# Kernel tuning notes

Hardware: AMD Instinct MI355X
Metric: run time of the kernel (lower is better)

## Reference

```python
import jax, jax.numpy as jnp
import numpy as np

KH, KW = 7, 7          # neighborhood kernel
NH = 8                 # num heads
PAD = (KW - 1) // 2    # circular pad along width


def setup_inputs() -> dict:
    key = jax.random.key(0)
    ks = jax.random.split(key, 6)
    B, H, W, C = 1, 180, 360, 256
    x = jax.random.normal(ks[0], (B, H, W, C), dtype=jnp.float32)
    w_qkv = jax.random.normal(ks[1], (C, 3 * C), dtype=jnp.float32) * 0.02
    b_qkv = jnp.zeros((3 * C,), dtype=jnp.float32)
    rpb = jax.random.normal(ks[2], (NH, 2 * KH - 1, 2 * KW - 1), dtype=jnp.float32) * 0.02
    w_proj = jax.random.normal(ks[3], (C, C), dtype=jnp.float32) * 0.02
    b_proj = jnp.zeros((C,), dtype=jnp.float32)
    return {"x": x, "w_qkv": w_qkv, "b_qkv": b_qkv, "rpb": rpb,
            "w_proj": w_proj, "b_proj": b_proj}


def _na2d(x, w_qkv, b_qkv, rpb, w_proj, b_proj):
    # x: [B, H, W, C] (already circularly padded along W)
    B, H, W, C = x.shape
    d = C // NH
    scale = d ** -0.5
    qkv = x @ w_qkv + b_qkv                       # [B,H,W,3C]
    qkv = qkv.reshape(B, H, W, 3, NH, d).transpose(3, 0, 4, 1, 2, 5)
    q, k, v = qkv[0] * scale, qkv[1], qkv[2]      # each [B,NH,H,W,d]

    # natten window start (clamped so the k x k window stays in-bounds)
    start_h = jnp.clip(jnp.arange(H) - (KH - 1) // 2, 0, H - KH)   # [H]
    start_w = jnp.clip(jnp.arange(W) - (KW - 1) // 2, 0, W - KW)   # [W]
    rel_h0 = start_h - jnp.arange(H) + (KH - 1)   # rpb row index base
    rel_w0 = start_w - jnp.arange(W) + (KW - 1)   # rpb col index base

    # scan over the KH*KW kernel offsets (honors the local-window sparsity;
    # never materializes [H,W,KH,KW,d] windows)
    oi, oj = jnp.meshgrid(jnp.arange(KH), jnp.arange(KW), indexing="ij")
    offs = jnp.stack([oi.ravel(), oj.ravel()], axis=-1)           # [KH*KW, 2]

    def score_body(_, off):
        kk = jnp.take(jnp.take(k, start_h + off[0], axis=2), start_w + off[1], axis=3)
        s = jnp.einsum("bnhwd,bnhwd->bnhw", q, kk)                # [B,NH,H,W]
        bias = rpb[:, rel_h0 + off[0], :][:, :, rel_w0 + off[1]]  # [NH,H,W]
        return None, s + bias[None]

    _, scores = jax.lax.scan(score_body, None, offs)              # [KH*KW,B,NH,H,W]
    attn = jax.nn.softmax(scores, axis=0)

    def out_body(acc, t):
        off, a = t
        vv = jnp.take(jnp.take(v, start_h + off[0], axis=2), start_w + off[1], axis=3)
        return acc + a[..., None] * vv, None

    out, _ = jax.lax.scan(out_body, jnp.zeros(q.shape, q.dtype), (offs, attn))
    out = out.transpose(0, 2, 3, 1, 4).reshape(B, H, W, C)        # merge heads
    return out @ w_proj + b_proj


def reference(x, w_qkv, b_qkv, rpb, w_proj, b_proj):
    # circular pad along width, neighborhood attention, crop back
    xp = jnp.pad(x, ((0, 0), (0, 0), (PAD, PAD), (0, 0)), mode="wrap")
    out = _na2d(xp, w_qkv, b_qkv, rpb, w_proj, b_proj)
    return out[:, :, PAD:out.shape[2] - PAD, :]
```

## Files before the change

### kernel.cpp

```cpp
#include <hip/hip_runtime.h>
#include <hip/hip_fp16.h>
#include <math.h>

#define H_DIM 180
#define W_DIM 360
#define CH    256
#define NHEAD 8
#define HD    32
#define MPIX  (H_DIM * W_DIM)
#define KDIM  256

typedef _Float16 f16x8 __attribute__((ext_vector_type(8)));
typedef _Float16 h2    __attribute__((ext_vector_type(2)));
typedef float    f32x4 __attribute__((ext_vector_type(4)));

#if __has_builtin(__builtin_amdgcn_fdot2)
#define HAS_FDOT2 1
#else
#define HAS_FDOT2 0
#endif

__device__ __forceinline__ h2 pack2(float a, float b) {
#if __has_builtin(__builtin_amdgcn_cvt_pkrtz)
    return __builtin_bit_cast(h2, __builtin_amdgcn_cvt_pkrtz(a, b));
#else
    h2 r; r.x = (_Float16)a; r.y = (_Float16)b; return r;
#endif
}

__global__ __launch_bounds__(256)
void convert_kernel(const float* __restrict__ X, const float* __restrict__ Wq,
                    const float* __restrict__ Wp, _Float16* __restrict__ Xh,
                    _Float16* __restrict__ Wqt, _Float16* __restrict__ Wpt)
{
    const int tid = blockIdx.x * 256 + threadIdx.x;
    if (blockIdx.y == 0) {
        const float4* X4 = reinterpret_cast<const float4*>(X);
        const float4 a = X4[tid * 2];
        const float4 b = X4[tid * 2 + 1];
        uint4 o;
        o.x = __builtin_bit_cast(unsigned, pack2(a.x, a.y));
        o.y = __builtin_bit_cast(unsigned, pack2(a.z, a.w));
        o.z = __builtin_bit_cast(unsigned, pack2(b.x, b.y));
        o.w = __builtin_bit_cast(unsigned, pack2(b.z, b.w));
        reinterpret_cast<uint4*>(Xh)[tid] = o;
    } else if (blockIdx.y == 1) {
        if (tid < 768 * 256) {
            const int n = tid >> 8, k = tid & 255;
            Wqt[tid] = (_Float16)Wq[k * 768 + n];
        }
    } else {
        if (tid < 256 * 256) {
            const int n = tid >> 8, k = tid & 255;
            Wpt[tid] = (_Float16)Wp[k * 256 + n];
        }
    }
}

template<int NB, int MODE>
__global__ __launch_bounds__(256)
void mfma_gemm_kernel(const _Float16* __restrict__ A,
                      const _Float16* __restrict__ Bt,
                      const float* __restrict__ bias,
                      _Float16* __restrict__ qo, _Float16* __restrict__ ko,
                      _Float16* __restrict__ vo, float* __restrict__ outf,
                      int M)
{
    __shared__ __align__(16) _Float16 Alds[128 * 64];
    __shared__ __align__(16) _Float16 Blds[128 * 64];

    const int tid  = threadIdx.x;
    const int wid  = tid >> 6;
    const int lane = tid & 63;
    const int bn   = blockIdx.x * 128;
    const int bm   = blockIdx.y * 128;
    const int wr   = wid >> 1;
    const int wc   = wid & 1;

    f32x4 acc[4][4] = {};

    const int srow  = lane >> 3;
    const int sunit = (lane & 7) * 16;

    for (int k0 = 0; k0 < KDIM; k0 += 64) {
        #pragma unroll
        for (int i = 0; i < 4; ++i) {
            const int chunk = i * 4 + wid;
            const int row   = chunk * 8 + srow;
            int am = bm + row;
            am = (am < M) ? am : (M - 1);
            const char* asrc = (const char*)(A + (size_t)am * KDIM + k0) + sunit;
            __builtin_amdgcn_global_load_lds(
                (const __attribute__((address_space(1))) void*)asrc,
                (__attribute__((address_space(3))) void*)((char*)Alds + chunk * 1024),
                16, 0, 0);
            const char* bsrc = (const char*)(Bt + (size_t)(bn + row) * KDIM + k0) + sunit;
            __builtin_amdgcn_global_load_lds(
                (const __attribute__((address_space(1))) void*)bsrc,
                (__attribute__((address_space(3))) void*)((char*)Blds + chunk * 1024),
                16, 0, 0);
        }
        __syncthreads();
        #pragma unroll
        for (int kk = 0; kk < 64; kk += 32) {
            const int ko2 = kk + (lane >> 4) * 8;
            f16x8 af[4], bf[4];
            #pragma unroll
            for (int t = 0; t < 4; ++t) {
                af[t] = *(const f16x8*)&Alds[(wr * 64 + t * 16 + (lane & 15)) * 64 + ko2];
                bf[t] = *(const f16x8*)&Blds[(wc * 64 + t * 16 + (lane & 15)) * 64 + ko2];
            }
            #pragma unroll
            for (int fi = 0; fi < 4; ++fi)
                #pragma unroll
                for (int fj = 0; fj < 4; ++fj)
                    acc[fi][fj] = __builtin_amdgcn_mfma_f32_16x16x32_f16(
                        af[fi], bf[fj], acc[fi][fj], 0, 0, 0);
        }
        __syncthreads();
    }

    const int lc  = lane & 15;
    const int lrb = (lane >> 4) * 4;
    if (MODE == 0) {
        const float scale = 0.17677669529663687f;
        _Float16* sw = Alds + wid * 640;
        const int row = lane >> 2;
        const int seg = lane & 3;
        #pragma unroll
        for (int fi = 0; fi < 4; ++fi) {
            #pragma unroll
            for (int fp = 0; fp < 2; ++fp) {
                #pragma unroll
                for (int ff = 0; ff < 2; ++ff) {
                    const int fj = fp * 2 + ff;
                    const int c = bn + wc * 64 + fj * 16 + lc;
                    const float bv = bias[c];
                    const float scl = ((c >> 8) == 0) ? scale : 1.0f;
                    #pragma unroll
                    for (int j = 0; j < 4; ++j)
                        sw[(lrb + j) * 34 + ff * 16 + lc] =
                            (_Float16)((acc[fi][fj][j] + bv) * scl);
                }
                const int c0 = bn + wc * 64 + fp * 32;
                const int which = c0 >> 8;
                const int head  = (c0 >> 5) & 7;
                _Float16* dst = (which == 0) ? qo : (which == 1) ? ko : vo;
                const int m = bm + wr * 64 + fi * 16 + row;
                f16x8 vv = *(const f16x8*)&sw[row * 34 + seg * 8];
                if (m < M)
                    *(f16x8*)&dst[((size_t)head * M + m) * HD + seg * 8] = vv;
            }
        }
    } else {
        #pragma unroll
        for (int fj = 0; fj < 4; ++fj) {
            const int c = bn + wc * 64 + fj * 16 + lc;
            const float bv = bias[c];
            #pragma unroll
            for (int fi = 0; fi < 4; ++fi) {
                #pragma unroll
                for (int j = 0; j < 4; ++j) {
                    const int m = bm + wr * 64 + fi * 16 + lrb + j;
                    if (m < M)
                        outf[(size_t)m * NB + c] = acc[fi][fj][j] + bv;
                }
            }
        }
    }
}

#define KROWS 14
#define KCOLS 38
#define KUNITS (KROWS * KCOLS * 4)
#define KUNITS_PAD 2304

__device__ __forceinline__ void stage_dma(const uint4* __restrict__ src,
                                          uint4* __restrict__ dstlds,
                                          int n, int r0, int w0, int tid)
{
    const int wid  = tid >> 6;
    const int lane = tid & 63;
    #pragma unroll
    for (int it = 0; it < 9; ++it) {
        const int u0 = it * 256 + wid * 64;
        const int u  = u0 + lane;
        const int row = u / (KCOLS * 4);
        const int rem = u - row * (KCOLS * 4);
        const int t   = rem / KCOLS;
        const int col = rem - t * KCOLS;
        int grow = r0 + row;
        if (grow > H_DIM - 1) grow = H_DIM - 1;
        int gcol = w0 - 3 + col;
        if (gcol < 0) gcol += W_DIM;
        else if (gcol >= W_DIM) gcol -= W_DIM;
        const size_t gidx = (((size_t)n * H_DIM + grow) * W_DIM + gcol) * 4 + t;
        __builtin_amdgcn_global_load_lds(
            (const __attribute__((address_space(1))) void*)(src + gidx),
            (__attribute__((address_space(3))) void*)(dstlds + u0), 16, 0, 0);
    }
}

__global__ __launch_bounds__(256)
void natten_attn_kernel(const _Float16* __restrict__ q,
                        const uint4* __restrict__ kb,
                        const uint4* __restrict__ vb,
                        const float* __restrict__ rpb,
                        _Float16* __restrict__ outh)
{
    __shared__ uint4 kvs[KUNITS_PAD];
    __shared__ float rpbs[169];

    const int tid = threadIdx.x;
    const int n  = blockIdx.z;
    const int w0 = blockIdx.x * 32;
    const int h0 = blockIdx.y * 8;

    int r0 = h0 - 3;
    if (r0 < 0) r0 = 0;
    if (r0 > H_DIM - 7) r0 = H_DIM - 7;

    if (tid < 169) rpbs[tid] = rpb[n * 169 + tid];

    const int hl = tid >> 5;
    const int wl = tid & 31;
    const int h = h0 + hl;
    const int w = w0 + wl;
    const bool valid = (h < H_DIM) && (w < W_DIM);

    const int ha = (h < H_DIM) ? h : H_DIM - 1;
    const int wa = (w < W_DIM) ? w : W_DIM - 1;
    const uint4* qp = reinterpret_cast<const uint4*>(
        q + ((size_t)n * MPIX + (size_t)ha * W_DIM + wa) * HD);
    uint4 q0 = qp[0], q1 = qp[1], q2 = qp[2], q3 = qp[3];

    stage_dma(kb, kvs, n, r0, w0, tid);
    __syncthreads();

    h2 qh[16];
    qh[0]  = __builtin_bit_cast(h2, q0.x); qh[1]  = __builtin_bit_cast(h2, q0.y);
    qh[2]  = __builtin_bit_cast(h2, q0.z); qh[3]  = __builtin_bit_cast(h2, q0.w);
    qh[4]  = __builtin_bit_cast(h2, q1.x); qh[5]  = __builtin_bit_cast(h2, q1.y);
    qh[6]  = __builtin_bit_cast(h2, q1.z); qh[7]  = __builtin_bit_cast(h2, q1.w);
    qh[8]  = __builtin_bit_cast(h2, q2.x); qh[9]  = __builtin_bit_cast(h2, q2.y);
    qh[10] = __builtin_bit_cast(h2, q2.z); qh[11] = __builtin_bit_cast(h2, q2.w);
    qh[12] = __builtin_bit_cast(h2, q3.x); qh[13] = __builtin_bit_cast(h2, q3.y);
    qh[14] = __builtin_bit_cast(h2, q3.z); qh[15] = __builtin_bit_cast(h2, q3.w);

    float sc[49];
    int ri0 = 0;

    if (valid) {
        int sh = h - 3;
        if (sh < 0) sh = 0;
        if (sh > H_DIM - 7) sh = H_DIM - 7;
        ri0 = sh - r0;
        const int rh0 = sh - h + 6;

        #pragma unroll
        for (int oi = 0; oi < 7; ++oi) {
            const int rb = (ri0 + oi) * (KCOLS * 4);
            #pragma unroll
            for (int oj = 0; oj < 7; ++oj) {
                const int base = rb + wl + oj;
                float d0 = 0.f, d1 = 0.f, d2 = 0.f, d3 = 0.f;
                const uint4 ku0 = kvs[base];
                const uint4 ku1 = kvs[base + KCOLS];
                const uint4 ku2 = kvs[base + 2 * KCOLS];
                const uint4 ku3 = kvs[base + 3 * KCOLS];
#if HAS_FDOT2
                d0 = __builtin_amdgcn_fdot2(__builtin_bit_cast(h2, ku0.x), qh[0],  d0, false);
                d1 = __builtin_amdgcn_fdot2(__builtin_bit_cast(h2, ku1.x), qh[4],  d1, false);
                d2 = __builtin_amdgcn_fdot2(__builtin_bit_cast(h2, ku2.x), qh[8],  d2, false);
                d3 = __builtin_amdgcn_fdot2(__builtin_bit_cast(h2, ku3.x), qh[12], d3, false);
                d0 = __builtin_amdgcn_fdot2(__builtin_bit_cast(h2, ku0.y), qh[1],  d0, false);
                d1 = __builtin_amdgcn_fdot2(__builtin_bit_cast(h2, ku1.y), qh[5],  d1, false);
                d2 = __builtin_amdgcn_fdot2(__builtin_bit_cast(h2, ku2.y), qh[9],  d2, false);
                d3 = __builtin_amdgcn_fdot2(__builtin_bit_cast(h2, ku3.y), qh[13], d3, false);
                d0 = __builtin_amdgcn_fdot2(__builtin_bit_cast(h2, ku0.z), qh[2],  d0, false);
                d1 = __builtin_amdgcn_fdot2(__builtin_bit_cast(h2, ku1.z), qh[6],  d1, false);
                d2 = __builtin_amdgcn_fdot2(__builtin_bit_cast(h2, ku2.z), qh[10], d2, false);
                d3 = __builtin_amdgcn_fdot2(__builtin_bit_cast(h2, ku3.z), qh[14], d3, false);
                d0 = __builtin_amdgcn_fdot2(__builtin_bit_cast(h2, ku0.w), qh[3],  d0, false);
                d1 = __builtin_amdgcn_fdot2(__builtin_bit_cast(h2, ku1.w), qh[7],  d1, false);
                d2 = __builtin_amdgcn_fdot2(__builtin_bit_cast(h2, ku2.w), qh[11], d2, false);
                d3 = __builtin_amdgcn_fdot2(__builtin_bit_cast(h2, ku3.w), qh[15], d3, false);
#else
                {
                    h2 a, b;
                    a = __builtin_bit_cast(h2, ku0.x); b = qh[0];
                    d0 += (float)a.x * (float)b.x + (float)a.y * (float)b.y;
                    a = __builtin_bit_cast(h2, ku0.y); b = qh[1];
                    d0 += (float)a.x * (float)b.x + (float)a.y * (float)b.y;
                    a = __builtin_bit_cast(h2, ku0.z); b = qh[2];
                    d0 += (float)a.x * (float)b.x + (float)a.y * (float)b.y;
                    a = __builtin_bit_cast(h2, ku0.w); b = qh[3];
                    d0 += (float)a.x * (float)b.x + (float)a.y * (float)b.y;
                    a = __builtin_bit_cast(h2, ku1.x); b = qh[4];
                    d1 += (float)a.x * (float)b.x + (float)a.y * (float)b.y;
                    a = __builtin_bit_cast(h2, ku1.y); b = qh[5];
                    d1 += (float)a.x * (float)b.x + (float)a.y * (float)b.y;
                    a = __builtin_bit_cast(h2, ku1.z); b = qh[6];
                    d1 += (float)a.x * (float)b.x + (float)a.y * (float)b.y;
                    a = __builtin_bit_cast(h2, ku1.w); b = qh[7];
                    d1 += (float)a.x * (float)b.x + (float)a.y * (float)b.y;
                    a = __builtin_bit_cast(h2, ku2.x); b = qh[8];
                    d2 += (float)a.x * (float)b.x + (float)a.y * (float)b.y;
                    a = __builtin_bit_cast(h2, ku2.y); b = qh[9];
                    d2 += (float)a.x * (float)b.x + (float)a.y * (float)b.y;
                    a = __builtin_bit_cast(h2, ku2.z); b = qh[10];
                    d2 += (float)a.x * (float)b.x + (float)a.y * (float)b.y;
                    a = __builtin_bit_cast(h2, ku2.w); b = qh[11];
                    d2 += (float)a.x * (float)b.x + (float)a.y * (float)b.y;
                    a = __builtin_bit_cast(h2, ku3.x); b = qh[12];
                    d3 += (float)a.x * (float)b.x + (float)a.y * (float)b.y;
                    a = __builtin_bit_cast(h2, ku3.y); b = qh[13];
                    d3 += (float)a.x * (float)b.x + (float)a.y * (float)b.y;
                    a = __builtin_bit_cast(h2, ku3.z); b = qh[14];
                    d3 += (float)a.x * (float)b.x + (float)a.y * (float)b.y;
                    a = __builtin_bit_cast(h2, ku3.w); b = qh[15];
                    d3 += (float)a.x * (float)b.x + (float)a.y * (float)b.y;
                }
#endif
                sc[oi * 7 + oj] = ((d0 + d1) + (d2 + d3))
                                + rpbs[(rh0 + oi) * 13 + 3 + oj];
            }
        }
    }
    __syncthreads();

    stage_dma(vb, kvs, n, r0, w0, tid);

    float inv = 0.f;
    if (valid) {
        float ssum = 0.f;
        #pragma unroll
        for (int i = 0; i < 49; ++i) { sc[i] = __expf(sc[i]); ssum += sc[i]; }
        inv = 1.f / ssum;
    }
    __syncthreads();

    if (!valid) return;

    float acc[32];
    #pragma unroll
    for (int t = 0; t < 32; ++t) acc[t] = 0.f;
    #pragma unroll
    for (int oi = 0; oi < 7; ++oi) {
        const int rb = (ri0 + oi) * (KCOLS * 4);
        #pragma unroll
        for (int oj = 0; oj < 7; ++oj) {
            const int base = rb + wl + oj;
            const float a = sc[oi * 7 + oj];
            #pragma unroll
            for (int t = 0; t < 4; ++t) {
                const uint4 vv = kvs[base + t * KCOLS];
                h2 v0 = __builtin_bit_cast(h2, vv.x);
                h2 v1 = __builtin_bit_cast(h2, vv.y);
                h2 v2 = __builtin_bit_cast(h2, vv.z);
                h2 v3 = __builtin_bit_cast(h2, vv.w);
                acc[t*8+0] += a * (float)v0.x; acc[t*8+1] += a * (float)v0.y;
                acc[t*8+2] += a * (float)v1.x; acc[t*8+3] += a * (float)v1.y;
                acc[t*8+4] += a * (float)v2.x; acc[t*8+5] += a * (float)v2.y;
                acc[t*8+6] += a * (float)v3.x; acc[t*8+7] += a * (float)v3.y;
            }
        }
    }

    uint4 o[4];
    #pragma unroll
    for (int t = 0; t < 4; ++t) {
        h2 p0 = { (_Float16)(acc[t*8+0] * inv), (_Float16)(acc[t*8+1] * inv) };
        h2 p1 = { (_Float16)(acc[t*8+2] * inv), (_Float16)(acc[t*8+3] * inv) };
        h2 p2 = { (_Float16)(acc[t*8+4] * inv), (_Float16)(acc[t*8+5] * inv) };
        h2 p3 = { (_Float16)(acc[t*8+6] * inv), (_Float16)(acc[t*8+7] * inv) };
        o[t].x = __builtin_bit_cast(unsigned, p0);
        o[t].y = __builtin_bit_cast(unsigned, p1);
        o[t].z = __builtin_bit_cast(unsigned, p2);
        o[t].w = __builtin_bit_cast(unsigned, p3);
    }
    uint4* op = reinterpret_cast<uint4*>(
        outh + (((size_t)h * W_DIM + w) * CH + n * HD));
    #pragma unroll
    for (int t = 0; t < 4; ++t) op[t] = o[t];
}

extern "C" void kernel_launch(void* const* d_in, const int* in_sizes, int n_in,
                              void* d_out, int out_size, void* d_ws, size_t ws_size,
                              hipStream_t stream)
{
    const float* x      = (const float*)d_in[0];
    const float* w_qkv  = (const float*)d_in[1];
    const float* b_qkv  = (const float*)d_in[2];
    const float* rpb    = (const float*)d_in[3];
    const float* w_proj = (const float*)d_in[4];
    const float* b_proj = (const float*)d_in[5];
    float* out = (float*)d_out;

    const int M = MPIX;
    const size_t nelem = (size_t)M * KDIM;

    _Float16* Xh  = (_Float16*)d_ws;
    _Float16* Wqt = Xh  + nelem;
    _Float16* Wpt = Wqt + 768 * 256;
    _Float16* qb  = Wpt + 256 * 256;
    _Float16* kb  = qb  + nelem;
    _Float16* vb  = kb  + nelem;
    _Float16* ah  = vb  + nelem;

    const size_t need = (5 * nelem + 768 * 256 + 256 * 256) * sizeof(_Float16);
    if (ws_size < need) return;

    dim3 blk(256);
    convert_kernel<<<dim3(8100, 3), blk, 0, stream>>>(x, w_qkv, w_proj, Xh, Wqt, Wpt);

    mfma_gemm_kernel<768, 0><<<dim3(6, 507), blk, 0, stream>>>(
        Xh, Wqt, b_qkv, qb, kb, vb, nullptr, M);

    natten_attn_kernel<<<dim3(12, 23, NHEAD), blk, 0, stream>>>(
        qb, (const uint4*)kb, (const uint4*)vb, rpb, ah);

    mfma_gemm_kernel<256, 1><<<dim3(2, 507), blk, 0, stream>>>(
        ah, Wpt, b_proj, nullptr, nullptr, nullptr, out, M);
}
```

Before: 197.9 us.

## Use square 16x16 attention tiles, fuse exp into scoring, pack scores to fp16

Changes the neighborhood-attention block tile from 8x32 to 16x16 pixels, which shrinks the staged K/V halo from 14x38 to 22x22 columns and cuts redundant LDS loads. The exponentials are computed inline during scoring and stored as packed fp16 pairs, which lowers register pressure, and the launch bounds now request 5 blocks per CU to raise occupancy. The trade-off is lower precision for the unnormalized softmax weights in fp16, plus a DMA loop whose last chunk overlaps the previous one.

```diff
diff --git a/kernel.cpp b/kernel.cpp
--- a/kernel.cpp
+++ b/kernel.cpp
@@ -170,10 +170,9 @@
     }
 }
 
-#define KROWS 14
-#define KCOLS 38
-#define KUNITS (KROWS * KCOLS * 4)
-#define KUNITS_PAD 2304
+#define KR 22
+#define KC 22
+#define KU (KR * KC * 4)
 
 __device__ __forceinline__ void stage_dma(const uint4* __restrict__ src,
                                           uint4* __restrict__ dstlds,
@@ -182,13 +181,14 @@
     const int wid  = tid >> 6;
     const int lane = tid & 63;
     #pragma unroll
-    for (int it = 0; it < 9; ++it) {
-        const int u0 = it * 256 + wid * 64;
+    for (int it = 0; it < 8; ++it) {
+        const int cb = (it == 7) ? (KU - 256) : it * 256;
+        const int u0 = cb + wid * 64;
         const int u  = u0 + lane;
-        const int row = u / (KCOLS * 4);
-        const int rem = u - row * (KCOLS * 4);
-        const int t   = rem / KCOLS;
-        const int col = rem - t * KCOLS;
+        const int row = u / (KC * 4);
+        const int rem = u - row * (KC * 4);
+        const int t   = rem / KC;
+        const int col = rem - t * KC;
         int grow = r0 + row;
         if (grow > H_DIM - 1) grow = H_DIM - 1;
         int gcol = w0 - 3 + col;
@@ -201,20 +201,20 @@
     }
 }
 
-__global__ __launch_bounds__(256)
+__global__ __launch_bounds__(256, 5)
 void natten_attn_kernel(const _Float16* __restrict__ q,
                         const uint4* __restrict__ kb,
                         const uint4* __restrict__ vb,
                         const float* __restrict__ rpb,
                         _Float16* __restrict__ outh)
 {
-    __shared__ uint4 kvs[KUNITS_PAD];
+    __shared__ uint4 kvs[KU];
     __shared__ float rpbs[169];
 
     const int tid = threadIdx.x;
     const int n  = blockIdx.z;
-    const int w0 = blockIdx.x * 32;
-    const int h0 = blockIdx.y * 8;
+    const int w0 = blockIdx.x * 16;
+    const int h0 = blockIdx.y * 16;
 
     int r0 = h0 - 3;
     if (r0 < 0) r0 = 0;
@@ -222,8 +222,8 @@
 
     if (tid < 169) rpbs[tid] = rpb[n * 169 + tid];
 
-    const int hl = tid >> 5;
-    const int wl = tid & 31;
+    const int hl = tid >> 4;
+    const int wl = tid & 15;
     const int h = h0 + hl;
     const int w = w0 + wl;
     const bool valid = (h < H_DIM) && (w < W_DIM);
@@ -247,7 +247,8 @@
     qh[12] = __builtin_bit_cast(h2, q3.x); qh[13] = __builtin_bit_cast(h2, q3.y);
     qh[14] = __builtin_bit_cast(h2, q3.z); qh[15] = __builtin_bit_cast(h2, q3.w);
 
-    float sc[49];
+    h2 sch[25];
+    float ssum = 0.f;
     int ri0 = 0;
 
     if (valid) {
@@ -257,17 +258,19 @@
         ri0 = sh - r0;
         const int rh0 = sh - h + 6;
 
+        float pend = 0.f;
         #pragma unroll
         for (int oi = 0; oi < 7; ++oi) {
-            const int rb = (ri0 + oi) * (KCOLS * 4);
+            const int rb = (ri0 + oi) * (KC * 4);
             #pragma unroll
             for (int oj = 0; oj < 7; ++oj) {
+                const int i = oi * 7 + oj;
                 const int base = rb + wl + oj;
                 float d0 = 0.f, d1 = 0.f, d2 = 0.f, d3 = 0.f;
                 const uint4 ku0 = kvs[base];
-                const uint4 ku1 = kvs[base + KCOLS];
-                const uint4 ku2 = kvs[base + 2 * KCOLS];
-                const uint4 ku3 = kvs[base + 3 * KCOLS];
+                const uint4 ku1 = kvs[base + KC];
+                const uint4 ku2 = kvs[base + 2 * KC];
+                const uint4 ku3 = kvs[base + 3 * KC];
 #if HAS_FDOT2
                 d0 = __builtin_amdgcn_fdot2(__builtin_bit_cast(h2, ku0.x), qh[0],  d0, false);
                 d1 = __builtin_amdgcn_fdot2(__builtin_bit_cast(h2, ku1.x), qh[4],  d1, false);
@@ -322,22 +325,21 @@
                     d3 += (float)a.x * (float)b.x + (float)a.y * (float)b.y;
                 }
 #endif
-                sc[oi * 7 + oj] = ((d0 + d1) + (d2 + d3))
-                                + rpbs[(rh0 + oi) * 13 + 3 + oj];
+                const float s = ((d0 + d1) + (d2 + d3))
+                              + rpbs[(rh0 + oi) * 13 + 3 + oj];
+                const float e = __expf(s);
+                ssum += e;
+                if (i & 1) sch[i >> 1] = pack2(pend, e);
+                else       pend = e;
             }
         }
+        sch[24] = pack2(pend, 0.f);
     }
     __syncthreads();
 
     stage_dma(vb, kvs, n, r0, w0, tid);
-
     float inv = 0.f;
-    if (valid) {
-        float ssum = 0.f;
-        #pragma unroll
-        for (int i = 0; i < 49; ++i) { sc[i] = __expf(sc[i]); ssum += sc[i]; }
-        inv = 1.f / ssum;
-    }
+    if (valid) inv = 1.f / ssum;
     __syncthreads();
 
     if (!valid) return;
@@ -347,14 +349,16 @@
     for (int t = 0; t < 32; ++t) acc[t] = 0.f;
     #pragma unroll
     for (int oi = 0; oi < 7; ++oi) {
-        const int rb = (ri0 + oi) * (KCOLS * 4);
+        const int rb = (ri0 + oi) * (KC * 4);
         #pragma unroll
         for (int oj = 0; oj < 7; ++oj) {
+            const int idx = oi * 7 + oj;
+            const h2 ee = sch[idx >> 1];
+            const float a = (idx & 1) ? (float)ee.y : (float)ee.x;
             const int base = rb + wl + oj;
-            const float a = sc[oi * 7 + oj];
             #pragma unroll
             for (int t = 0; t < 4; ++t) {
-                const uint4 vv = kvs[base + t * KCOLS];
+                const uint4 vv = kvs[base + t * KC];
                 h2 v0 = __builtin_bit_cast(h2, vv.x);
                 h2 v1 = __builtin_bit_cast(h2, vv.y);
                 h2 v2 = __builtin_bit_cast(h2, vv.z);
@@ -417,7 +421,8 @@
     mfma_gemm_kernel<768, 0><<<dim3(6, 507), blk, 0, stream>>>(
         Xh, Wqt, b_qkv, qb, kb, vb, nullptr, M);
 
-    natten_attn_kernel<<<dim3(12, 23, NHEAD), blk, 0, stream>>>(
+    natten_attn_kernel<<<dim3((W_DIM + 15) / 16, (H_DIM + 15) / 16, NHEAD),
+                         blk, 0, stream>>>(
         qb, (const uint4*)kb, (const uint4*)vb, rpb, ah);
 
     mfma_gemm_kernel<256, 1><<<dim3(2, 507), blk, 0, stream>>>(
```

New measurement: 777.0 us. 3.93x slower.
